# Kernel optimization log

Measured on AMD Instinct MI355X. Metric: run time of the kernel, lower is better.

## Reference

```python
import jax, jax.numpy as jnp
import numpy as np

RATIO = 2          # BigVGAN Activation1d up/down ratio
K_FILT = 12        # int(6 * ratio // 2) * 2
DILATIONS = (1, 3, 5)


def _kaiser_sinc_filter1d(cutoff, half_width, kernel_size):
    # Faithful port of BigVGAN's kaiser_sinc_filter1d (even kernel path).
    half_size = kernel_size // 2
    delta_f = 4.0 * half_width
    A = 2.285 * (half_size - 1) * np.pi * delta_f + 7.95
    if A > 50.0:
        beta = 0.1102 * (A - 8.7)
    elif A >= 21.0:
        beta = 0.5842 * (A - 21.0) ** 0.4 + 0.07886 * (A - 21.0)
    else:
        beta = 0.0
    window = np.kaiser(kernel_size, beta)              # periodic=False
    time = np.arange(-half_size, half_size) + 0.5       # even kernel size
    filt = 2.0 * cutoff * window * np.sinc(2.0 * cutoff * time)
    filt = filt / filt.sum()
    return jnp.asarray(filt, dtype=jnp.float32)

FILT = _kaiser_sinc_filter1d(0.5 / RATIO, 0.6 / RATIO, K_FILT)


def _depthwise1d(x, filt, stride, lhs_dilation, padding):
    # x: (B, T, C), filt: (k,) shared across channels (depthwise)
    C = x.shape[-1]
    kern = jnp.tile(filt[:, None, None], (1, 1, C))  # (k, 1, C)
    return jax.lax.conv_general_dilated(
        x, kern, window_strides=(stride,), padding=padding,
        lhs_dilation=(lhs_dilation,), feature_group_count=C,
        dimension_numbers=('NLC', 'LIO', 'NLC'))


def upsample2(x):
    # BigVGAN UpSample1d(ratio=2): replicate pad -> conv_transpose -> crop
    pad = K_FILT // RATIO - 1                       # 5
    pad_left = pad * RATIO + (K_FILT - RATIO) // 2  # 15
    pad_right = pad * RATIO + (K_FILT - RATIO + 1) // 2  # 15
    x = jnp.pad(x, ((0, 0), (pad, pad), (0, 0)), mode='edge')
    # conv_transpose(stride=r) == lhs-dilated conv with full padding
    # (filter is symmetric, so no flip needed)
    y = RATIO * _depthwise1d(x, FILT, 1, RATIO, [(K_FILT - 1, K_FILT - 1)])
    return y[:, pad_left:-pad_right, :]  # (B, 2T, C)


def downsample2(x):
    # BigVGAN DownSample1d(ratio=2) == LowPassFilter1d(stride=2)
    pad_left = K_FILT // 2 - 1  # 5 (even kernel)
    pad_right = K_FILT // 2     # 6
    x = jnp.pad(x, ((0, 0), (pad_left, pad_right), (0, 0)), mode='edge')
    return _depthwise1d(x, FILT, RATIO, 1, 'VALID')  # (B, T, C)


def snake(x, log_alpha):
    # alpha_logscale=True: alpha = exp(param); x + (1/alpha) sin^2(alpha x)
    alpha = jnp.exp(log_alpha)  # (C,), broadcasts over (B, T, C)
    return x + (1.0 / (alpha + 1e-9)) * jnp.square(jnp.sin(alpha * x))


def act1d(x, log_alpha):
    return downsample2(snake(upsample2(x), log_alpha))


def wn_conv(x, v, g, b, dilation):
    # weight-norm: kernel = v / ||v||_(0,1) * g, then SAME dilated conv
    norm = jnp.linalg.norm(v, axis=(0, 1))[None, None, :]  # (1,1,Cout)
    kern = (v / norm) * g  # (k, Cin, Cout)
    y = jax.lax.conv_general_dilated(
        x, kern, window_strides=(1,), padding='SAME',
        rhs_dilation=(dilation,), dimension_numbers=('NLC', 'LIO', 'NLC'))
    return y + b


def setup_inputs() -> dict:
    key = jax.random.key(0)
    ks = jax.random.split(key, 7)
    B, T, C, K = 4, 8192, 512, 3
    n = len(DILATIONS)
    x = jax.random.normal(ks[0], (B, T, C), dtype=jnp.float32)
    v1 = jax.random.normal(ks[1], (n, K, C, C), dtype=jnp.float32)
    g1 = jax.random.uniform(ks[2], (n, 1, 1, C), dtype=jnp.float32)
    b1 = 0.01 * jax.random.normal(ks[3], (n, C), dtype=jnp.float32)
    v2 = jax.random.normal(ks[4], (n, K, C, C), dtype=jnp.float32)
    g2 = jax.random.uniform(ks[5], (n, 1, 1, C), dtype=jnp.float32)
    b2 = 0.01 * jax.random.normal(ks[6], (n, C), dtype=jnp.float32)
    alphas = jnp.zeros((2 * n, C), dtype=jnp.float32)  # log-alpha init 0
    return {'x': x, 'v1': v1, 'g1': g1, 'b1': b1,
            'v2': v2, 'g2': g2, 'b2': b2, 'alphas': alphas}


def reference(x, v1, g1, b1, v2, g2, b2, alphas):
    for i, d in enumerate(DILATIONS):
        xt = act1d(x, alphas[2 * i])
        xt = wn_conv(xt, v1[i], g1[i], b1[i], d)
        xt = act1d(xt, alphas[2 * i + 1])
        xt = wn_conv(xt, v2[i], g2[i], b2[i], 1)
        x = xt + x
    return x
```

## Files before the change

### kernel.cpp

```cpp
#include <hip/hip_runtime.h>
#include <math.h>

#define TLEN   8192
#define CCH    512
#define NBATCH 4
#define GUARD_B 8
#define GUARD_T 16
#define XROWS  (TLEN + GUARD_B + GUARD_T)

typedef __attribute__((ext_vector_type(8))) short short8;
typedef __attribute__((ext_vector_type(4))) float f32x4;

struct Filt { float f[12]; };

#define MFMA16(a, b, c) __builtin_amdgcn_mfma_f32_16x16x32_bf16(a, b, c, 0, 0, 0)

__device__ __forceinline__ unsigned short f2bf(float f) {
  unsigned u = __float_as_uint(f);
  unsigned r = (u + 0x7fffu + ((u >> 16) & 1u)) >> 16;
  return (unsigned short)r;
}

__device__ __forceinline__ float bf2f(unsigned short u) {
  return __uint_as_float((unsigned)u << 16);
}

__device__ __forceinline__ float fast_sin(float x) {
  float r = x * 0.15915494309189535f;
  r -= floorf(r);
  return __builtin_amdgcn_sinf(r);
}

__device__ __forceinline__ float snake1(float u, float a, float rcp) {
  float s = fast_sin(a * u);
  return fmaf(rcp * s, s, u);
}

__device__ __forceinline__ void gload16(const void* g, void* l) {
  __builtin_amdgcn_global_load_lds(
      (const __attribute__((address_space(1))) unsigned int*)g,
      (__attribute__((address_space(3))) unsigned int*)l, 16, 0, 0);
}

__global__ __launch_bounds__(256)
void normp_k(const float* __restrict__ v1, const float* __restrict__ v2,
             float* __restrict__ part) {
  __shared__ float red[256];
  const int c  = blockIdx.x;
  const int cc = blockIdx.y;
  const int jc = blockIdx.z;
  const int col = threadIdx.x & 63;
  const int js  = threadIdx.x >> 6;
  const int co = cc * 64 + col;
  const float* v = (c < 3) ? v1 + (size_t)c * 3 * CCH * CCH
                           : v2 + (size_t)(c - 3) * 3 * CCH * CCH;
  const int j0 = jc * 64 + js * 16;
  float s = 0.f;
  #pragma unroll
  for (int jj = 0; jj < 16; ++jj) {
    float w = v[(size_t)(j0 + jj) * CCH + co];
    s = fmaf(w, w, s);
  }
  red[threadIdx.x] = s;
  __syncthreads();
  if (threadIdx.x < 64) {
    float t = red[threadIdx.x] + red[threadIdx.x + 64] +
              red[threadIdx.x + 128] + red[threadIdx.x + 192];
    part[(size_t)(c * CCH + co) * 24 + jc] = t;
  }
}

__global__ __launch_bounds__(256)
void fin_k(const float* __restrict__ part, const float* __restrict__ g1,
           const float* __restrict__ g2, float* __restrict__ scl) {
  const int i = blockIdx.x * 256 + threadIdx.x;
  const int c = i >> 9, co = i & 511;
  float s = 0.f;
  #pragma unroll
  for (int jc = 0; jc < 24; ++jc) s += part[(size_t)i * 24 + jc];
  const float g = (c < 3) ? g1[c * CCH + co] : g2[(c - 3) * CCH + co];
  scl[i] = g / sqrtf(s);
}

__global__ __launch_bounds__(512)
void zguard_k(unsigned short* __restrict__ xb) {
  const int b = blockIdx.x / 24;
  const int g = blockIdx.x % 24;
  const int row = (g < 8) ? g : (TLEN + g);
  xb[((size_t)b * XROWS + row) * CCH + threadIdx.x] = 0;
}

__global__ __launch_bounds__(256)
void wprep_k(const float* __restrict__ v1, const float* __restrict__ v2,
             const float* __restrict__ scl, unsigned short* __restrict__ wp) {
  const int gtid = blockIdx.x * 256 + threadIdx.x;
  const int lane = gtid & 63;
  const int gw = gtid >> 6;
  const int c  = gw / 1536;
  int r = gw - c * 1536;
  const int tap = r >> 9;  r &= 511;
  const int cib = r >> 6;  r &= 63;
  const int cob = r >> 4;
  const int cb  = r & 15;
  const int nf = cb >> 1, kk = cb & 1;
  const int co  = cob * 128 + nf * 16 + (lane & 15);
  const int ci0 = cib * 64 + kk * 32 + (lane >> 4) * 8;
  const float* v = (c < 3) ? v1 + (size_t)c * 3 * CCH * CCH
                           : v2 + (size_t)(c - 3) * 3 * CCH * CCH;
  const float s = scl[c * CCH + co];
  unsigned short o[8];
  #pragma unroll
  for (int j = 0; j < 8; ++j) {
    float w = v[((size_t)tap * CCH + ci0 + j) * CCH + co] * s;
    o[j] = f2bf(w);
  }
  *reinterpret_cast<short8*>(wp + (size_t)gw * 512 + lane * 8) =
      *reinterpret_cast<const short8*>(o);
}

template<int INBF>
__global__ __launch_bounds__(256)
void act_k(const void* __restrict__ xin, unsigned short* __restrict__ y,
           const float* __restrict__ la, Filt F) {
  const int idx = blockIdx.x * 256 + threadIdx.x;
  const int c  = (idx & 127) << 2;
  const int ts = (idx >> 7) & 2047;
  const int b  = idx >> 18;
  const int t0 = ts * 4;

  auto ldrow = [&](int row) -> f32x4 {
    if constexpr (INBF) {
      const unsigned short* p =
          (const unsigned short*)xin + ((size_t)b * TLEN + row) * CCH + c;
      ushort4 u = *reinterpret_cast<const ushort4*>(p);
      f32x4 r;
      r[0] = bf2f(u.x); r[1] = bf2f(u.y); r[2] = bf2f(u.z); r[3] = bf2f(u.w);
      return r;
    } else {
      const float* p = (const float*)xin + ((size_t)b * TLEN + row) * CCH + c;
      return *reinterpret_cast<const f32x4*>(p);
    }
  };

  float av[4], rv[4];
  #pragma unroll
  for (int ch = 0; ch < 4; ++ch) {
    av[ch] = expf(la[c + ch]);
    rv[ch] = 1.f / (av[ch] + 1e-9f);
  }

  float acc[4][4];

  if (ts >= 2 && ts <= 2045) {
    f32x4 xw[14];
    #pragma unroll
    for (int j = 0; j < 14; ++j) xw[j] = ldrow(t0 - 5 + j);

    #pragma unroll
    for (int ch = 0; ch < 4; ++ch) {
      float s[18];
      #pragma unroll
      for (int mi = 0; mi < 18; ++mi) {
        float u = 0.f;
        if (mi & 1) {
          const int base = (mi - 5) / 2 + 2;
          #pragma unroll
          for (int r = 0; r < 6; ++r) u = fmaf(F.f[2*r], xw[base + r][ch], u);
        } else {
          const int base = (mi - 6) / 2 + 3;
          #pragma unroll
          for (int r = 0; r < 6; ++r) u = fmaf(F.f[2*r+1], xw[base + r][ch], u);
        }
        u *= 2.f;
        s[mi] = snake1(u, av[ch], rv[ch]);
      }
      #pragma unroll
      for (int tt = 0; tt < 4; ++tt) {
        float a = 0.f;
        #pragma unroll
        for (int k = 0; k < 12; ++k) a = fmaf(F.f[k], s[2*tt + k], a);
        acc[tt][ch] = a;
      }
    }
  } else {
    #pragma unroll
    for (int tt = 0; tt < 4; ++tt) {
      const int t = t0 + tt;
      float a0=0.f, a1=0.f, a2=0.f, a3=0.f;
      for (int k = 0; k < 12; ++k) {
        int m  = 2*t + k - 5;
        int mc = m < 0 ? 0 : (m > 2*TLEN - 1 ? 2*TLEN - 1 : m);
        int tp = mc >> 1;
        int odd = mc & 1;
        float u0=0.f,u1=0.f,u2=0.f,u3=0.f;
        #pragma unroll
        for (int r = 0; r < 6; ++r) {
          int i  = odd ? (tp + r - 2) : (tp + r - 3);
          int ic = i < 0 ? 0 : (i > TLEN - 1 ? TLEN - 1 : i);
          float tap = odd ? F.f[2*r+1] : F.f[2*r];
          f32x4 xv = ldrow(ic);
          u0 = fmaf(tap, xv[0], u0); u1 = fmaf(tap, xv[1], u1);
          u2 = fmaf(tap, xv[2], u2); u3 = fmaf(tap, xv[3], u3);
        }
        u0 *= 2.f; u1 *= 2.f; u2 *= 2.f; u3 *= 2.f;
        const float fk = F.f[k];
        a0 = fmaf(fk, snake1(u0,av[0],rv[0]), a0);
        a1 = fmaf(fk, snake1(u1,av[1],rv[1]), a1);
        a2 = fmaf(fk, snake1(u2,av[2],rv[2]), a2);
        a3 = fmaf(fk, snake1(u3,av[3],rv[3]), a3);
      }
      acc[tt][0]=a0; acc[tt][1]=a1; acc[tt][2]=a2; acc[tt][3]=a3;
    }
  }

  #pragma unroll
  for (int tt = 0; tt < 4; ++tt) {
    ushort4 o;
    o.x = f2bf(acc[tt][0]); o.y = f2bf(acc[tt][1]);
    o.z = f2bf(acc[tt][2]); o.w = f2bf(acc[tt][3]);
    *reinterpret_cast<ushort4*>(
        y + ((size_t)b * XROWS + GUARD_B + t0 + tt) * CCH + c) = o;
  }
}

template<int DIL, int OB>
__global__ __launch_bounds__(512)
void convm_k(const unsigned short* __restrict__ xb,
             const unsigned short* __restrict__ wp,
             const float* __restrict__ bia,
             const float* __restrict__ res,
             float* __restrict__ outf,
             unsigned short* __restrict__ outb) {
  __shared__ unsigned short As[272 * 64];
  __shared__ unsigned short Bs[2][16 * 512];

  const int tid  = threadIdx.x;
  const int lane = tid & 63;
  const int wid  = tid >> 6;
  const int wr = wid >> 1, wc = wid & 1;

  const int l   = (blockIdx.x & 7) * 64 + (blockIdx.x >> 3);
  const int coB = l & 3;
  const int tb  = l >> 2;
  const int b   = tb >> 5;
  const int t0  = (tb & 31) * 256;
  const int co0 = coB * 128;

  const int qq = lane >> 4;
  const int r0 = lane & 15;

  const int a_r = lane >> 3;
  const int a_c = (lane & 7) ^ a_r;
  const unsigned short* xrow0 =
      xb + ((size_t)b * XROWS + GUARD_B + t0 - DIL) * CCH;

  f32x4 acc[4][4] = {};

  auto stageA = [&](int cib) {
    #pragma unroll
    for (int u = 0; u < 5; ++u) {
      const int i = wid + u * 8;
      if (i < 34) {
        const unsigned short* g =
            xrow0 + (size_t)(8 * i + a_r) * CCH + cib * 64 + a_c * 8;
        gload16(g, &As[i * 512]);
      }
    }
  };
  auto stageB = [&](int tap, int cib, int buf) {
    #pragma unroll
    for (int u = 0; u < 2; ++u) {
      const int cb = wid * 2 + u;
      const unsigned short* g =
          wp + ((((size_t)(tap * 8 + cib) * 4 + coB) * 16 + cb) * 512) + lane * 8;
      gload16(g, &Bs[buf][cb * 512]);
    }
  };
  auto compute = [&](int tap, int pb) {
    const int rowbase = tap * DIL + wr * 64 + r0;
    const int xr = (tap * DIL + r0) & 7;
    #pragma unroll
    for (int kk = 0; kk < 2; ++kk) {
      const int coff = 8 * ((kk * 4 + qq) ^ xr);
      short8 af[4], bf[4];
      #pragma unroll
      for (int i = 0; i < 4; ++i)
        af[i] = *reinterpret_cast<const short8*>(
            &As[(rowbase + i * 16) * 64 + coff]);
      #pragma unroll
      for (int j = 0; j < 4; ++j)
        bf[j] = *reinterpret_cast<const short8*>(
            &Bs[pb][((wc * 4 + j) * 2 + kk) * 512 + lane * 8]);
      #pragma unroll
      for (int i = 0; i < 4; ++i)
        #pragma unroll
        for (int j = 0; j < 4; ++j)
          acc[i][j] = MFMA16(af[i], bf[j], acc[i][j]);
    }
  };

  stageA(0);
  stageB(0, 0, 0);
  __syncthreads();

  int pb = 0;
  for (int cib = 0; cib < 8; ++cib) {
    #pragma unroll
    for (int tap = 0; tap < 3; ++tap) {
      if (tap < 2) {
        stageB(tap + 1, cib, pb ^ 1);
      } else if (cib < 7) {
        stageB(0, cib + 1, pb ^ 1);
      }
      compute(tap, pb);
      if (tap == 2 && cib < 7) {
        __syncthreads();
        stageA(cib + 1);
      }
      __syncthreads();
      pb ^= 1;
    }
  }

  #pragma unroll
  for (int j = 0; j < 4; ++j) {
    const int co = co0 + (wc * 4 + j) * 16 + r0;
    const float bv = bia[co];
    #pragma unroll
    for (int i = 0; i < 4; ++i) {
      const int t = t0 + wr * 64 + i * 16 + qq * 4;
      #pragma unroll
      for (int e = 0; e < 4; ++e) {
        const size_t off = ((size_t)b * TLEN + t + e) * CCH + co;
        float o = acc[i][j][e] + bv;
        if constexpr (OB) {
          outb[off] = f2bf(o);
        } else {
          if (res) o += res[off];
          outf[off] = o;
        }
      }
    }
  }
}

static double bessel_i0(double x) {
  double t = 1.0, s = 1.0, q = x * x * 0.25;
  for (int k = 1; k < 64; ++k) {
    t *= q / ((double)k * (double)k);
    s += t;
    if (t < 1e-18 * s) break;
  }
  return s;
}

static void make_filter(Filt* F) {
  const double cutoff = 0.25, hw = 0.3;
  const int ks = 12, half = 6;
  const double A = 2.285 * (half - 1) * M_PI * (4.0 * hw) + 7.95;
  double beta;
  if (A > 50.0)       beta = 0.1102 * (A - 8.7);
  else if (A >= 21.0) beta = 0.5842 * pow(A - 21.0, 0.4) + 0.07886 * (A - 21.0);
  else                beta = 0.0;
  const double i0b = bessel_i0(beta);
  double f[12], sum = 0.0;
  for (int n = 0; n < 12; ++n) {
    double rr = 2.0 * n / (ks - 1) - 1.0;
    double w  = bessel_i0(beta * sqrt(fmax(0.0, 1.0 - rr * rr))) / i0b;
    double tm = (double)(n - half) + 0.5;
    double sx = 2.0 * cutoff * tm;
    double snc = (sx == 0.0) ? 1.0 : sin(M_PI * sx) / (M_PI * sx);
    f[n] = 2.0 * cutoff * w * snc;
    sum += f[n];
  }
  for (int n = 0; n < 12; ++n) F->f[n] = (float)(f[n] / sum);
}

extern "C" void kernel_launch(void* const* d_in, const int* in_sizes, int n_in,
                              void* d_out, int out_size, void* d_ws, size_t ws_size,
                              hipStream_t stream) {
  (void)in_sizes; (void)n_in; (void)out_size; (void)ws_size;
  const float* x  = (const float*)d_in[0];
  const float* v1 = (const float*)d_in[1];
  const float* g1 = (const float*)d_in[2];
  const float* b1 = (const float*)d_in[3];
  const float* v2 = (const float*)d_in[4];
  const float* g2 = (const float*)d_in[5];
  const float* b2 = (const float*)d_in[6];
  const float* al = (const float*)d_in[7];
  float* out = (float*)d_out;

  const size_t N = (size_t)NBATCH * TLEN * CCH;
  unsigned short* wb1  = (unsigned short*)d_ws;
  unsigned short* xbuf = wb1 + N;
  unsigned short* wp   = xbuf + (size_t)NBATCH * XROWS * CCH;
  float* part = (float*)(wp + (size_t)6 * 3 * CCH * CCH);
  float* scl  = part + (size_t)6 * CCH * 24;

  Filt F;
  make_filter(&F);

  zguard_k<<<96, 512, 0, stream>>>(xbuf);
  normp_k<<<dim3(6, 8, 24), 256, 0, stream>>>(v1, v2, part);
  fin_k<<<12, 256, 0, stream>>>(part, g1, g2, scl);
  wprep_k<<<2304, 256, 0, stream>>>(v1, v2, scl, wp);

  const int cgrid = NBATCH * (TLEN / 256) * 4;
  const int nblk_act = (NBATCH * 2048 * 128) / 256;
  const size_t wsz = (size_t)3 * CCH * CCH;

  for (int i = 0; i < 3; ++i) {
    const float* xsrc = (i == 0) ? x : out;
    act_k<0><<<nblk_act, 256, 0, stream>>>(xsrc, xbuf, al + (size_t)(2 * i) * CCH, F);
    if (i == 0)
      convm_k<1, 1><<<cgrid, 512, 0, stream>>>(xbuf, wp + 0 * wsz, b1 + 0 * CCH,
                                               nullptr, nullptr, wb1);
    else if (i == 1)
      convm_k<3, 1><<<cgrid, 512, 0, stream>>>(xbuf, wp + 1 * wsz, b1 + 1 * CCH,
                                               nullptr, nullptr, wb1);
    else
      convm_k<5, 1><<<cgrid, 512, 0, stream>>>(xbuf, wp + 2 * wsz, b1 + 2 * CCH,
                                               nullptr, nullptr, wb1);
    act_k<1><<<nblk_act, 256, 0, stream>>>(wb1, xbuf, al + (size_t)(2 * i + 1) * CCH, F);
    convm_k<1, 0><<<cgrid, 512, 0, stream>>>(xbuf, wp + (3 + i) * wsz, b2 + i * CCH,
                                             xsrc, out, nullptr);
  }
}
```

Baseline: 723.0 us.

## Rewrite conv GEMM with 256x256 tiles and ping-pong double-buffered pipeline

The conv kernel now uses 256-row by 256-channel output tiles per block instead of 256x128, which halves the grid and doubles the accumulators per wave. A and B are staged per (tap, cib) step into double-buffered LDS using manual s_barrier and vmcnt waits, so global loads overlap with MFMA work. It also raises MFMA priority with setprio and repacks the weights to match the new tile order. More registers per wave and the hand-placed waitcnt/barrier schedule add risk to occupancy and to correctness of the synchronisation.

Measured after the change: 685.8 us. 5.1% less time.

```diff
diff --git a/kernel.cpp b/kernel.cpp
--- a/kernel.cpp
+++ b/kernel.cpp
@@ -14,6 +14,8 @@
 struct Filt { float f[12]; };
 
 #define MFMA16(a, b, c) __builtin_amdgcn_mfma_f32_16x16x32_bf16(a, b, c, 0, 0, 0)
+#define BARRIER() asm volatile("s_barrier" ::: "memory")
+#define VMCNT(n)  asm volatile("s_waitcnt vmcnt(" #n ")" ::: "memory")
 
 __device__ __forceinline__ unsigned short f2bf(float f) {
   unsigned u = __float_as_uint(f);
@@ -97,21 +99,22 @@
   const int lane = gtid & 63;
   const int gw = gtid >> 6;
   const int c  = gw / 1536;
-  int r = gw - c * 1536;
-  const int tap = r >> 9;  r &= 511;
-  const int cib = r >> 6;  r &= 63;
-  const int cob = r >> 4;
-  const int cb  = r & 15;
+  const int r  = gw - c * 1536;
+  const int s  = r >> 6;
+  const int r2 = r & 63;
+  const int coT = r2 >> 5;
+  const int cb  = r2 & 31;
+  const int tap = s % 3, cib = s / 3;
   const int nf = cb >> 1, kk = cb & 1;
-  const int co  = cob * 128 + nf * 16 + (lane & 15);
+  const int co  = coT * 256 + nf * 16 + (lane & 15);
   const int ci0 = cib * 64 + kk * 32 + (lane >> 4) * 8;
   const float* v = (c < 3) ? v1 + (size_t)c * 3 * CCH * CCH
                            : v2 + (size_t)(c - 3) * 3 * CCH * CCH;
-  const float s = scl[c * CCH + co];
+  const float sc = scl[c * CCH + co];
   unsigned short o[8];
   #pragma unroll
   for (int j = 0; j < 8; ++j) {
-    float w = v[((size_t)tap * CCH + ci0 + j) * CCH + co] * s;
+    float w = v[((size_t)tap * CCH + ci0 + j) * CCH + co] * sc;
     o[j] = f2bf(w);
   }
   *reinterpret_cast<short8*>(wp + (size_t)gw * 512 + lane * 8) =
@@ -224,111 +227,131 @@
 }
 
 template<int DIL, int OB>
-__global__ __launch_bounds__(512)
+__global__ __launch_bounds__(512, 2)
 void convm_k(const unsigned short* __restrict__ xb,
              const unsigned short* __restrict__ wp,
              const float* __restrict__ bia,
              const float* __restrict__ res,
              float* __restrict__ outf,
              unsigned short* __restrict__ outb) {
-  __shared__ unsigned short As[272 * 64];
-  __shared__ unsigned short Bs[2][16 * 512];
+  __shared__ unsigned short Abuf[2][2][128 * 64];
+  __shared__ unsigned short Bbuf[2][2][16 * 512];
 
   const int tid  = threadIdx.x;
   const int lane = tid & 63;
   const int wid  = tid >> 6;
-  const int wr = wid >> 1, wc = wid & 1;
-
-  const int l   = (blockIdx.x & 7) * 64 + (blockIdx.x >> 3);
-  const int coB = l & 3;
-  const int tb  = l >> 2;
+  const int wr   = wid >> 2;
+  const int wcn  = wid & 3;
+
+  const int l   = (blockIdx.x & 7) * 32 + (blockIdx.x >> 3);
+  const int coT = l & 1;
+  const int tb  = l >> 1;
   const int b   = tb >> 5;
   const int t0  = (tb & 31) * 256;
-  const int co0 = coB * 128;
+  const int co0 = coT * 256;
 
   const int qq = lane >> 4;
   const int r0 = lane & 15;
+  const int xr = r0 & 7;
 
   const int a_r = lane >> 3;
   const int a_c = (lane & 7) ^ a_r;
+
   const unsigned short* xrow0 =
       xb + ((size_t)b * XROWS + GUARD_B + t0 - DIL) * CCH;
-
-  f32x4 acc[4][4] = {};
-
-  auto stageA = [&](int cib) {
-    #pragma unroll
-    for (int u = 0; u < 5; ++u) {
-      const int i = wid + u * 8;
-      if (i < 34) {
-        const unsigned short* g =
-            xrow0 + (size_t)(8 * i + a_r) * CCH + cib * 64 + a_c * 8;
-        gload16(g, &As[i * 512]);
+  const unsigned short* wpc = wp + (size_t)coT * 32 * 512 + lane * 8;
+
+  f32x4 acc[8][4] = {};
+  short8 bfr[4][2];
+
+  auto stA = [&](int s, int h) {
+    const int tap = s % 3, cib = s / 3;
+    const unsigned short* base =
+        xrow0 + (size_t)(tap * DIL + h * 128) * CCH + cib * 64;
+    #pragma unroll
+    for (int u = 0; u < 2; ++u) {
+      const int i = wid * 2 + u;
+      gload16(base + (size_t)(8 * i + a_r) * CCH + a_c * 8,
+              &Abuf[s & 1][h][i * 512]);
+    }
+  };
+  auto stB = [&](int s, int h) {
+    #pragma unroll
+    for (int u = 0; u < 2; ++u) {
+      const int cbl = wid * 2 + u;
+      gload16(wpc + ((size_t)s * 64 + h * 16 + cbl) * 512,
+              &Bbuf[s & 1][h][cbl * 512]);
+    }
+  };
+  auto ldB = [&](int slot) {
+    const int hb = wcn >> 1;
+    #pragma unroll
+    for (int j = 0; j < 4; ++j)
+      #pragma unroll
+      for (int kk = 0; kk < 2; ++kk) {
+        const int chunk = ((wcn & 1) * 4 + j) * 2 + kk;
+        bfr[j][kk] = *reinterpret_cast<const short8*>(
+            &Bbuf[slot][hb][chunk * 512 + lane * 8]);
       }
-    }
-  };
-  auto stageB = [&](int tap, int cib, int buf) {
-    #pragma unroll
-    for (int u = 0; u < 2; ++u) {
-      const int cb = wid * 2 + u;
-      const unsigned short* g =
-          wp + ((((size_t)(tap * 8 + cib) * 4 + coB) * 16 + cb) * 512) + lane * 8;
-      gload16(g, &Bs[buf][cb * 512]);
-    }
-  };
-  auto compute = [&](int tap, int pb) {
-    const int rowbase = tap * DIL + wr * 64 + r0;
-    const int xr = (tap * DIL + r0) & 7;
-    #pragma unroll
-    for (int kk = 0; kk < 2; ++kk) {
-      const int coff = 8 * ((kk * 4 + qq) ^ xr);
-      short8 af[4], bf[4];
-      #pragma unroll
-      for (int i = 0; i < 4; ++i)
-        af[i] = *reinterpret_cast<const short8*>(
-            &As[(rowbase + i * 16) * 64 + coff]);
-      #pragma unroll
-      for (int j = 0; j < 4; ++j)
-        bf[j] = *reinterpret_cast<const short8*>(
-            &Bs[pb][((wc * 4 + j) * 2 + kk) * 512 + lane * 8]);
-      #pragma unroll
-      for (int i = 0; i < 4; ++i)
+  };
+  auto ldA = [&](int slot, int q, short8 (&af)[2][2]) {
+    #pragma unroll
+    for (int e = 0; e < 2; ++e) {
+      const int row = q * 32 + e * 16 + r0;
+      #pragma unroll
+      for (int kk = 0; kk < 2; ++kk)
+        af[e][kk] = *reinterpret_cast<const short8*>(
+            &Abuf[slot][wr][row * 64 + ((kk * 4 + qq) ^ xr) * 8]);
+    }
+  };
+  auto mma = [&](int q, short8 (&af)[2][2]) {
+    __builtin_amdgcn_s_setprio(1);
+    #pragma unroll
+    for (int kk = 0; kk < 2; ++kk)
+      #pragma unroll
+      for (int e = 0; e < 2; ++e)
         #pragma unroll
         for (int j = 0; j < 4; ++j)
-          acc[i][j] = MFMA16(af[i], bf[j], acc[i][j]);
-    }
-  };
-
-  stageA(0);
-  stageB(0, 0, 0);
-  __syncthreads();
-
-  int pb = 0;
-  for (int cib = 0; cib < 8; ++cib) {
-    #pragma unroll
-    for (int tap = 0; tap < 3; ++tap) {
-      if (tap < 2) {
-        stageB(tap + 1, cib, pb ^ 1);
-      } else if (cib < 7) {
-        stageB(0, cib + 1, pb ^ 1);
-      }
-      compute(tap, pb);
-      if (tap == 2 && cib < 7) {
-        __syncthreads();
-        stageA(cib + 1);
-      }
-      __syncthreads();
-      pb ^= 1;
-    }
+          acc[q * 2 + e][j] = MFMA16(af[e][kk], bfr[j][kk], acc[q * 2 + e][j]);
+    __builtin_amdgcn_s_setprio(0);
+  };
+
+  stA(0, 0); stA(0, 1);
+  stB(0, 0); stB(0, 1);
+  stB(1, 0); stB(1, 1);
+  VMCNT(4);
+  BARRIER();
+
+  for (int m = 0; m < 12; ++m) {
+    const int s0 = 2 * m, s1 = 2 * m + 1;
+    short8 af[2][2];
+    ldB(0); ldA(0, 0, af); stA(s1, 0);
+    BARRIER(); mma(0, af); BARRIER();
+    ldA(0, 1, af); stA(s1, 1);
+    BARRIER(); mma(1, af); BARRIER();
+    ldA(0, 2, af); if (m < 11) stB(s0 + 2, 0);
+    BARRIER(); mma(2, af); BARRIER();
+    ldA(0, 3, af);
+    if (m < 11) { stB(s0 + 2, 1); VMCNT(4); } else { VMCNT(0); }
+    BARRIER(); mma(3, af); BARRIER();
+    ldB(1); ldA(1, 0, af); if (m < 11) stA(s0 + 2, 0);
+    BARRIER(); mma(0, af); BARRIER();
+    ldA(1, 1, af); if (m < 11) stA(s0 + 2, 1);
+    BARRIER(); mma(1, af); BARRIER();
+    ldA(1, 2, af); if (m < 11) stB(s1 + 2, 0);
+    BARRIER(); mma(2, af); BARRIER();
+    ldA(1, 3, af);
+    if (m < 11) { stB(s1 + 2, 1); VMCNT(4); }
+    BARRIER(); mma(3, af); BARRIER();
   }
 
   #pragma unroll
   for (int j = 0; j < 4; ++j) {
-    const int co = co0 + (wc * 4 + j) * 16 + r0;
+    const int co = co0 + wcn * 64 + j * 16 + r0;
     const float bv = bia[co];
     #pragma unroll
-    for (int i = 0; i < 4; ++i) {
-      const int t = t0 + wr * 64 + i * 16 + qq * 4;
+    for (int i = 0; i < 8; ++i) {
+      const int t = t0 + wr * 128 + i * 16 + qq * 4;
       #pragma unroll
       for (int e = 0; e < 4; ++e) {
         const size_t off = ((size_t)b * TLEN + t + e) * CCH + co;
@@ -405,7 +428,7 @@
   fin_k<<<12, 256, 0, stream>>>(part, g1, g2, scl);
   wprep_k<<<2304, 256, 0, stream>>>(v1, v2, scl, wp);
 
-  const int cgrid = NBATCH * (TLEN / 256) * 4;
+  const int cgrid = NBATCH * (TLEN / 256) * 2;
   const int nblk_act = (NBATCH * 2048 * 128) / 256;
   const size_t wsz = (size_t)3 * CCH * CCH;
 
```
